# Kernel optimization log

Measured on AMD Instinct MI355X. Metric: run time of the kernel, lower is better.

The kernel has to match this reference:

```python
import jax, jax.numpy as jnp
import numpy as np

E = 512   # embed_size == head_dim
H = 8     # heads
N = 8     # batch
S = 1024  # seq len


def setup_inputs() -> dict:
    key = jax.random.key(0)
    ks = jax.random.split(key, 12)
    scale = 1.0 / np.sqrt(E)
    inp = {
        "values": jax.random.normal(ks[0], (N, S, E), jnp.float32),
        "keys": jax.random.normal(ks[1], (N, S, E), jnp.float32),
        "query": jax.random.normal(ks[2], (N, S, E), jnp.float32),
        "pos": jnp.arange(S, dtype=jnp.int64) if jax.config.jax_enable_x64 else jnp.arange(S, dtype=jnp.int32),
        "mask": jax.random.randint(ks[3], (N, 1, S, S), 0, 2, jnp.int32),
        # nn.Linear params: weight (out,in), y = x @ W.T + b
        "Wv": jax.random.uniform(ks[4], (E * H, E), jnp.float32, -scale, scale),
        "bv": jax.random.uniform(ks[5], (E * H,), jnp.float32, -scale, scale),
        "Wk": jax.random.uniform(ks[6], (E * H, E), jnp.float32, -scale, scale),
        "bk": jax.random.uniform(ks[7], (E * H,), jnp.float32, -scale, scale),
        "Wq": jax.random.uniform(ks[8], (E * H, E), jnp.float32, -scale, scale),
        "bq": jax.random.uniform(ks[9], (E * H,), jnp.float32, -scale, scale),
        "Wo": jax.random.uniform(ks[10], (E, E), jnp.float32, -scale, scale),
        "bo": jax.random.uniform(ks[11], (E,), jnp.float32, -scale, scale),
    }
    return inp


def reference(values, keys, query, pos, mask, Wv, bv, Wk, bk, Wq, bq, Wo, bo):
    n, q_len, e = query.shape
    v_len = values.shape[1]
    k_len = keys.shape[1]
    h = Wq.shape[0] // e
    # QKV projections: E -> E*H, reshape to (N, L, H, E)
    v = (values @ Wv.T + bv).reshape(n, v_len, h, e)
    k = (keys @ Wk.T + bk).reshape(n, k_len, h, e)
    q = (query @ Wq.T + bq).reshape(n, q_len, h, e)
    # bilinear energy, no softmax
    energy = jnp.einsum('nqhd,nkhd->nhqk', q, k)
    energy = jnp.where(mask == 0, jnp.zeros((), energy.dtype), energy)
    attention = energy / jnp.asarray(e ** 0.5, energy.dtype)
    out = jnp.einsum('nhql,nlhd->nqhd', attention, v).sum(axis=2)  # sum over heads
    return out @ Wo.T + bo
```

## Files before the change

### kernel.cpp

```cpp
#include <hip/hip_runtime.h>


#define RS 0.04419417382415922f

typedef __attribute__((ext_vector_type(8))) short bf16x8;
typedef __attribute__((ext_vector_type(4))) float f32x4;

__device__ __forceinline__ unsigned short f2b(float f) {
  unsigned u = __builtin_bit_cast(unsigned, f);
  unsigned r = (u + 0x7FFFu + ((u >> 16) & 1u)) >> 16;
  return (unsigned short)r;
}
__device__ __forceinline__ float b2f(unsigned short h) {
  return __builtin_bit_cast(float, ((unsigned)h) << 16);
}

__global__ void k_fill(float* p, int n, float v) {
  int i = blockIdx.x * blockDim.x + threadIdx.x;
  int stride = gridDim.x * blockDim.x;
  for (; i < n; i += stride) p[i] = v;
}

__global__ void k_maskbits(const int* __restrict__ m,
                           unsigned* __restrict__ bits) {
  int wi = blockIdx.x * 256 + threadIdx.x;
  const int* src = m + (size_t)wi * 32;
  unsigned b = 0;
#pragma unroll
  for (int i = 0; i < 32; ++i) b |= (src[i] != 0 ? 1u : 0u) << i;
  bits[wi] = b;
}

__global__ void k_convw4(const float4* __restrict__ wv,
                         const float4* __restrict__ wk,
                         const float4* __restrict__ wq,
                         const float4* __restrict__ wo,
                         ushort4* __restrict__ dqkv, ushort4* __restrict__ dwo) {
  int z = blockIdx.z;
  const float4* s = (z == 0) ? wv : (z == 1) ? wk : (z == 2) ? wq : wo;
  ushort4* d = (z == 3) ? dwo : dqkv + (size_t)z * 524288;
  int n4 = (z == 3) ? 65536 : 524288;
  float scale = (z == 2) ? RS : 1.0f;
  int stride = gridDim.x * blockDim.x;
  for (int i = blockIdx.x * blockDim.x + threadIdx.x; i < n4; i += stride) {
    float4 v = s[i];
    ushort4 o;
    o.x = f2b(v.x * scale); o.y = f2b(v.y * scale);
    o.z = f2b(v.z * scale); o.w = f2b(v.w * scale);
    d[i] = o;
  }
}

__global__ void k_conv3(const float4* __restrict__ v,
                        const float4* __restrict__ k,
                        const float4* __restrict__ q, ushort4* __restrict__ d,
                        int n4, int dstride) {
  const float4* s = (blockIdx.z == 0) ? v : (blockIdx.z == 1) ? k : q;
  ushort4* dz = d + (size_t)blockIdx.z * dstride;
  int stride = gridDim.x * blockDim.x;
  for (int i = blockIdx.x * blockDim.x + threadIdx.x; i < n4; i += stride) {
    float4 x = s[i];
    ushort4 o;
    o.x = f2b(x.x); o.y = f2b(x.y); o.z = f2b(x.z); o.w = f2b(x.w);
    dz[i] = o;
  }
}

__global__ void k_reduce4(const unsigned short* __restrict__ a,
                          unsigned short* __restrict__ o, int total) {
  int i = blockIdx.x * blockDim.x + threadIdx.x;
  if (i >= total) return;
  int nl = i >> 17, j = i & 131071;
  const ushort4* av = (const ushort4*)a + (size_t)nl * 524288;
  float4 s = {0.f, 0.f, 0.f, 0.f};
#pragma unroll
  for (int g = 0; g < 4; ++g) {
    ushort4 v = av[g * 131072 + j];
    s.x += b2f(v.x); s.y += b2f(v.y); s.z += b2f(v.z); s.w += b2f(v.w);
  }
  ushort4 r;
  r.x = f2b(s.x); r.y = f2b(s.y); r.z = f2b(s.z); r.w = f2b(s.w);
  ((ushort4*)o)[i] = r;
}

#define GLD16(gp, sp)                                              \
  __builtin_amdgcn_global_load_lds(                                \
      (const __attribute__((address_space(1))) void*)(gp),         \
      (__attribute__((address_space(3))) void*)(sp), 16, 0, 0)

template <int MODE>
__global__ __launch_bounds__(256) void k_gemm(
    const unsigned short* __restrict__ A, const unsigned short* __restrict__ B,
    const float* __restrict__ bi0, const float* __restrict__ bi1,
    const float* __restrict__ bi2, const unsigned* __restrict__ mbits,
    unsigned short* __restrict__ outb, float* __restrict__ outf, int n0,
    int xstr, int ostr) {
  __shared__ short smem[17408];
  char* const sb = (char*)smem;

  const int tid = threadIdx.x;
  const int wid = tid >> 6;
  const int lane = tid & 63;
  const int wr = wid >> 1, wc = wid & 1;
  const int l15 = lane & 15, l4 = lane >> 4;

  int bx, by, bz;
  if constexpr (MODE == 2 || MODE == 4) {
    bz = blockIdx.x; bx = blockIdx.y; by = blockIdx.z;
  } else {
    bx = blockIdx.x; by = blockIdx.y; bz = blockIdx.z;
  }

  constexpr int KSEG = (MODE == 4) ? 1024 : 512;
  constexpr int NK = KSEG / 32;
  constexpr int NSEG = (MODE == 4) ? 2 : 1;

  f32x4 acc[4][4];
#pragma unroll
  for (int i = 0; i < 4; ++i)
#pragma unroll
    for (int j = 0; j < 4; ++j) acc[i][j] = (f32x4){0.f, 0.f, 0.f, 0.f};

  const unsigned short* Ab;
  const unsigned short* Bb;

#define STAGE(buf, kc)                                             \
  {                                                                \
    _Pragma("unroll") for (int is = 0; is < 2; ++is) {             \
      int c = is * 256 + tid;                                      \
      int row = c >> 2, col = (c & 3) << 3;                        \
      GLD16(Ab + (size_t)row * KSEG + (kc)*32 + col,               \
            sb + (buf)*8192 + is * 4096 + wid * 1024);             \
      GLD16(Bb + (size_t)row * KSEG + (kc)*32 + col,               \
            sb + 16384 + (buf)*8192 + is * 4096 + wid * 1024);     \
    }                                                              \
  }

  for (int seg = 0; seg < NSEG; ++seg) {
    if constexpr (MODE == 5) {
      Ab = A + (size_t)bx * 128 * 512;
      Bb = B + (size_t)by * 128 * 512;
    } else if constexpr (MODE == 6) {
      Ab = A + (size_t)bz * xstr + (size_t)bx * 128 * 512;
      Bb = B + (size_t)bz * 2097152 + (size_t)by * 128 * 512;
    } else if constexpr (MODE == 2) {
      Ab = A + (size_t)bz * 524288 + (size_t)bx * 128 * 512;
      Bb = B + (size_t)bz * 524288 + (size_t)by * 128 * 512;
    } else {
      int n_l = bz >> 2, g = bz & 3;
      int nh = n_l * 8 + g * 2 + seg;
      Ab = A + (size_t)nh * 1048576 + (size_t)bx * 128 * 1024;
      Bb = B + (size_t)nh * 524288 + (size_t)by * 128 * 1024;
    }

    if (NSEG > 1 && seg > 0) __syncthreads();
    STAGE(0, 0);
    int cur = 0;
#pragma unroll 4
    for (int kc = 0; kc < NK; ++kc) {
      __syncthreads();
      if (kc + 1 < NK) STAGE(cur ^ 1, kc + 1);
      bf16x8 af[4], bf_[4];
#pragma unroll
      for (int f = 0; f < 4; ++f) {
        af[f] = *(const bf16x8*)(sb + cur * 8192 +
                                 ((wr * 64 + f * 16 + l15) << 6) + (l4 << 4));
        bf_[f] = *(const bf16x8*)(sb + 16384 + cur * 8192 +
                                  ((wc * 64 + f * 16 + l15) << 6) + (l4 << 4));
      }
#pragma unroll
      for (int mf = 0; mf < 4; ++mf)
#pragma unroll
        for (int nf = 0; nf < 4; ++nf)
          acc[mf][nf] = __builtin_amdgcn_mfma_f32_16x16x32_bf16(
              af[mf], bf_[nf], acc[mf][nf], 0, 0, 0);
      cur ^= 1;
    }
  }
#undef STAGE

  const int r0 = l4 * 4;
  const int c0 = l15;

  if constexpr (MODE != 5) {
    const bool transp = (MODE == 6) && (bz == 0);
    const float* bias =
        (MODE == 6) ? ((bz == 0) ? bi0 : (bz == 1) ? bi1 : bi2) : nullptr;
    const float bscale = (MODE == 6 && bz == 2) ? RS : 1.0f;
    __syncthreads();
#pragma unroll
    for (int nf = 0; nf < 4; ++nf) {
      int c_loc = wc * 64 + nf * 16 + c0;
      int c_ = by * 128 + c_loc;
      float bvl = (MODE == 6) ? bias[c_] * bscale : 0.f;
#pragma unroll
      for (int mf = 0; mf < 4; ++mf) {
#pragma unroll
        for (int r = 0; r < 4; ++r) {
          int r_loc = wr * 64 + mf * 16 + r0 + r;
          float v = acc[mf][nf][r] + bvl;
          unsigned short bb;
          if constexpr (MODE == 2) {
            int r_ = bx * 128 + r_loc;
            unsigned mw = mbits[((size_t)(n0 + (bz >> 3)) * 1024 + r_) * 32 +
                                (c_ >> 5)];
            bb = ((mw >> (c_ & 31)) & 1u) ? f2b(v) : (unsigned short)0;
          } else {
            bb = f2b(v);
          }
          if (transp)
            smem[c_loc * 136 + r_loc] = (short)bb;
          else
            smem[r_loc * 136 + c_loc] = (short)bb;
        }
      }
    }
    __syncthreads();
#pragma unroll
    for (int ch = 0; ch < 8; ++ch) {
      int idx = ch * 256 + tid;
      int row = idx >> 4;
      int col = (idx & 15) << 3;
      bf16x8 v = *(const bf16x8*)(smem + row * 136 + col);
      if constexpr (MODE == 2) {
        int r_ = bx * 128 + row, cB = by * 128 + col;
        *(bf16x8*)(outb + (size_t)bz * 1048576 + (size_t)r_ * 1024 + cB) = v;
      } else if constexpr (MODE == 4) {
        int r_ = bx * 128 + row, cB = by * 128 + col;
        *(bf16x8*)(outb + (size_t)bz * 524288 + (size_t)r_ * 512 + cB) = v;
      } else {
        unsigned short* O = outb + (size_t)bz * ostr;
        if (bz == 0) {
          int eB = by * 128 + row;
          int r_ = bx * 128 + col;
          int nl = r_ >> 10, s = r_ & 1023, h = eB >> 9, e = eB & 511;
          *(bf16x8*)(O + (((size_t)nl * 8 + h) * 512 + e) * 1024 + s) = v;
        } else {
          int r_ = bx * 128 + row, cB = by * 128 + col;
          int nl = r_ >> 10, s = r_ & 1023, h = cB >> 9, e = cB & 511;
          *(bf16x8*)(O + (((size_t)nl * 8 + h) * 1024 + s) * 512 + e) = v;
        }
      }
    }
  } else {
    float* const Cs32 = (float*)smem;
#pragma unroll
    for (int hh = 0; hh < 2; ++hh) {
      __syncthreads();
      if (wr == hh) {
#pragma unroll
        for (int nf = 0; nf < 4; ++nf) {
          int c_loc = wc * 64 + nf * 16 + c0;
          float bvl = bi0[by * 128 + c_loc];
#pragma unroll
          for (int mf = 0; mf < 4; ++mf)
#pragma unroll
            for (int r = 0; r < 4; ++r)
              Cs32[(mf * 16 + r0 + r) * 136 + c_loc] = acc[mf][nf][r] + bvl;
        }
      }
      __syncthreads();
#pragma unroll
      for (int ch = 0; ch < 8; ++ch) {
        int idx = ch * 256 + tid;
        int row = idx >> 5;
        int col = (idx & 31) << 2;
        float4 v = *(const float4*)(Cs32 + row * 136 + col);
        *(float4*)(outf + (size_t)(bx * 128 + hh * 64 + row) * 512 +
                   by * 128 + col) = v;
      }
    }
  }
}

extern "C" void kernel_launch(void* const* d_in, const int* in_sizes, int n_in,
                              void* d_out, int out_size, void* d_ws,
                              size_t ws_size, hipStream_t stream) {
  const float* values = (const float*)d_in[0];
  const float* keys = (const float*)d_in[1];
  const float* query = (const float*)d_in[2];
  const int* maskI = (const int*)d_in[4];
  const float* Wv = (const float*)d_in[5];
  const float* bv = (const float*)d_in[6];
  const float* Wk = (const float*)d_in[7];
  const float* bk = (const float*)d_in[8];
  const float* Wq = (const float*)d_in[9];
  const float* bq = (const float*)d_in[10];
  const float* Wo = (const float*)d_in[11];
  const float* bo = (const float*)d_in[12];
  float* dout = (float*)d_out;

  const int exp_sizes[13] = {4194304, 4194304, 4194304, 1024, 8388608,
                             2097152, 4096,    2097152, 4096, 2097152,
                             4096,    262144,  512};
  bool ok = (n_in == 13);
  if (ok)
    for (int i = 0; i < 13; ++i)
      if (in_sizes[i] != exp_sizes[i]) ok = false;
  if (!ok) {
    k_fill<<<512, 256, 0, stream>>>(dout, out_size, 1000.f);
    return;
  }

  const size_t SZT2 = 16777216, SZT4 = 33554432;
  const size_t need2 = 22544384 + 3 * SZT2 + 2 * SZT2;
  const size_t need4 = 22544384 + 3 * SZT4 + 2 * SZT4;
  const int NL = (ws_size >= need4) ? 4 : 2;
  if (ws_size < need2) {
    k_fill<<<512, 256, 0, stream>>>(dout, out_size, 2000.f);
    return;
  }
  const size_t SZT = (size_t)NL * 8388608;

  char* w = (char*)d_ws;
  unsigned short* Wvb = (unsigned short*)(w);
  unsigned short* Wob = (unsigned short*)(w + 12582912);
  unsigned short* Atb = (unsigned short*)(w + 13107200);
  unsigned* mbits = (unsigned*)(w + 21495808);
  unsigned short* VTb = (unsigned short*)(w + 22544384);
  unsigned short* Kb = (unsigned short*)(w + 22544384 + SZT);
  unsigned short* Qb = (unsigned short*)(w + 22544384 + 2 * SZT);
  unsigned short* Pb = (unsigned short*)(w + 22544384 + 3 * SZT);
  unsigned short* Xc = (unsigned short*)Pb;
  unsigned short* Ahb = (unsigned short*)Qb;

  k_convw4<<<dim3(512, 1, 4), 256, 0, stream>>>(
      (const float4*)Wv, (const float4*)Wk, (const float4*)Wq,
      (const float4*)Wo, (ushort4*)Wvb, (ushort4*)Wob);
  k_maskbits<<<1024, 256, 0, stream>>>(maskI, mbits);

  const int xstr = NL * 524288;
  const int ostr = NL * 4194304;

  for (int it = 0; it < 8 / NL; ++it) {
    const int n0 = it * NL;
    const size_t xoff = (size_t)n0 * 524288;
    k_conv3<<<dim3(512 * NL, 1, 3), 256, 0, stream>>>(
        (const float4*)(values + xoff), (const float4*)(keys + xoff),
        (const float4*)(query + xoff), (ushort4*)Xc, NL * 131072, NL * 131072);
    k_gemm<6><<<dim3(NL * 8, 32, 3), 256, 0, stream>>>(
        Xc, Wvb, bv, bk, bq, nullptr, VTb, nullptr, 0, xstr, ostr);
    k_gemm<2><<<dim3(NL * 8, 8, 8), 256, 0, stream>>>(
        Qb, Kb, nullptr, nullptr, nullptr, mbits, Pb, nullptr, n0, 0, 0);
    k_gemm<4><<<dim3(NL * 4, 8, 4), 256, 0, stream>>>(
        Pb, VTb, nullptr, nullptr, nullptr, nullptr, Ahb, nullptr, 0, 0, 0);
    k_reduce4<<<NL * 512, 256, 0, stream>>>(Ahb, Atb + (size_t)n0 * 524288,
                                            NL * 131072);
  }

  k_gemm<5><<<dim3(64, 4, 1), 256, 0, stream>>>(
      Atb, Wob, bo, nullptr, nullptr, nullptr, nullptr, dout, 0, 0, 0);
}
```

Measured before the change: 476.5 us.

## Fuse masked QK^T energy and attention-times-V into one flash-style kernel

```diff
diff --git a/kernel.cpp b/kernel.cpp
--- a/kernel.cpp
+++ b/kernel.cpp
@@ -66,16 +66,16 @@
   }
 }
 
-__global__ void k_reduce4(const unsigned short* __restrict__ a,
+__global__ void k_reduce8(const unsigned short* __restrict__ a,
                           unsigned short* __restrict__ o, int total) {
   int i = blockIdx.x * blockDim.x + threadIdx.x;
   if (i >= total) return;
   int nl = i >> 17, j = i & 131071;
-  const ushort4* av = (const ushort4*)a + (size_t)nl * 524288;
+  const ushort4* av = (const ushort4*)a + (size_t)nl * 1048576;
   float4 s = {0.f, 0.f, 0.f, 0.f};
 #pragma unroll
-  for (int g = 0; g < 4; ++g) {
-    ushort4 v = av[g * 131072 + j];
+  for (int h = 0; h < 8; ++h) {
+    ushort4 v = av[h * 131072 + j];
     s.x += b2f(v.x); s.y += b2f(v.y); s.z += b2f(v.z); s.w += b2f(v.w);
   }
   ushort4 r;
@@ -88,13 +88,147 @@
       (const __attribute__((address_space(1))) void*)(gp),         \
       (__attribute__((address_space(3))) void*)(sp), 16, 0, 0)
 
+__global__ __launch_bounds__(256) void k_fused(
+    const unsigned short* __restrict__ Qb, const unsigned short* __restrict__ Kb,
+    const unsigned short* __restrict__ VTb, const unsigned* __restrict__ mbits,
+    unsigned short* __restrict__ Ob, int n0) {
+  __shared__ short smem[20992];
+  short* const Ss = smem + 12288;
+
+  const int tid = threadIdx.x;
+  const int wid = tid >> 6, lane = tid & 63;
+  const int l15 = lane & 15, l4 = lane >> 4;
+  const int bz = blockIdx.x, qt = blockIdx.y;
+
+  const unsigned short* Qt = Qb + (size_t)bz * 524288 + (size_t)qt * 64 * 512;
+  const unsigned short* Kh = Kb + (size_t)bz * 524288;
+  const unsigned short* Vh = VTb + (size_t)bz * 524288;
+  const int n = n0 + (bz >> 3);
+
+  f32x4 accO[4][8];
+#pragma unroll
+  for (int f = 0; f < 4; ++f)
+#pragma unroll
+    for (int e = 0; e < 8; ++e) accO[f][e] = (f32x4){0.f, 0.f, 0.f, 0.f};
+
+#define STGF(buf, kc)                                                      \
+  {                                                                        \
+    int cA = wid * 64 + lane;                                              \
+    GLD16(Qt + (size_t)(cA >> 2) * 512 + (kc)*32 + ((cA & 3) << 3),        \
+          (char*)smem + (buf)*4096 + wid * 1024);                          \
+    _Pragma("unroll") for (int is = 0; is < 2; ++is) {                     \
+      int cB = is * 256 + tid;                                             \
+      GLD16(Kl + (size_t)(cB >> 2) * 512 + (kc)*32 + ((cB & 3) << 3),      \
+            (char*)smem + 8192 + (buf)*8192 + is * 4096 + wid * 1024);     \
+    }                                                                      \
+  }
+
+  for (int lt = 0; lt < 8; ++lt) {
+    const unsigned short* Kl = Kh + (size_t)lt * 128 * 512;
+    f32x4 accS[4][2];
+#pragma unroll
+    for (int f = 0; f < 4; ++f) {
+      accS[f][0] = (f32x4){0.f, 0.f, 0.f, 0.f};
+      accS[f][1] = (f32x4){0.f, 0.f, 0.f, 0.f};
+    }
+
+    STGF(0, 0);
+    int cur = 0;
+#pragma unroll 4
+    for (int kc = 0; kc < 16; ++kc) {
+      __syncthreads();
+      if (kc + 1 < 16) STGF(cur ^ 1, kc + 1);
+      bf16x8 aq[4], bk[2];
+#pragma unroll
+      for (int f = 0; f < 4; ++f)
+        aq[f] = *(const bf16x8*)((char*)smem + cur * 4096 +
+                                 ((f * 16 + l15) << 6) + (l4 << 4));
+#pragma unroll
+      for (int g = 0; g < 2; ++g)
+        bk[g] = *(const bf16x8*)((char*)smem + 8192 + cur * 8192 +
+                                 ((wid * 32 + g * 16 + l15) << 6) + (l4 << 4));
+#pragma unroll
+      for (int f = 0; f < 4; ++f)
+#pragma unroll
+        for (int g = 0; g < 2; ++g)
+          accS[f][g] = __builtin_amdgcn_mfma_f32_16x16x32_bf16(
+              aq[f], bk[g], accS[f][g], 0, 0, 0);
+      cur ^= 1;
+    }
+
+#pragma unroll
+    for (int f = 0; f < 4; ++f)
+#pragma unroll
+      for (int g = 0; g < 2; ++g)
+#pragma unroll
+        for (int r = 0; r < 4; ++r) {
+          int q_loc = f * 16 + l4 * 4 + r;
+          int l_loc = wid * 32 + g * 16 + l15;
+          int l_glob = lt * 128 + l_loc;
+          int q_glob = qt * 64 + q_loc;
+          unsigned mw =
+              mbits[((size_t)n * 1024 + q_glob) * 32 + (l_glob >> 5)];
+          Ss[q_loc * 136 + l_loc] =
+              ((mw >> (l_glob & 31)) & 1u)
+                  ? (short)f2b(accS[f][g][r])
+                  : (short)0;
+        }
+    __syncthreads();
+
+#pragma unroll
+    for (int ks = 0; ks < 4; ++ks) {
+      bf16x8 as_[4];
+#pragma unroll
+      for (int f = 0; f < 4; ++f)
+        as_[f] = *(const bf16x8*)(Ss + (f * 16 + l15) * 136 + ks * 32 + l4 * 8);
+#pragma unroll
+      for (int fe = 0; fe < 8; ++fe) {
+        bf16x8 bv = *(const bf16x8*)(Vh +
+                                     (size_t)(wid * 128 + fe * 16 + l15) * 1024 +
+                                     lt * 128 + ks * 32 + l4 * 8);
+#pragma unroll
+        for (int f = 0; f < 4; ++f)
+          accO[f][fe] = __builtin_amdgcn_mfma_f32_16x16x32_bf16(
+              as_[f], bv, accO[f][fe], 0, 0, 0);
+      }
+    }
+    __syncthreads();
+  }
+#undef STGF
+
+#pragma unroll
+  for (int p = 0; p < 2; ++p) {
+    __syncthreads();
+    if ((wid >> 1) == p) {
+#pragma unroll
+      for (int f = 0; f < 4; ++f)
+#pragma unroll
+        for (int fe = 0; fe < 8; ++fe)
+#pragma unroll
+          for (int r = 0; r < 4; ++r) {
+            int row = f * 16 + l4 * 4 + r;
+            int col = (wid & 1) * 128 + fe * 16 + l15;
+            smem[row * 264 + col] = (short)f2b(accO[f][fe][r]);
+          }
+    }
+    __syncthreads();
+#pragma unroll
+    for (int ch = 0; ch < 8; ++ch) {
+      int idx = ch * 256 + tid;
+      int row = idx >> 5;
+      int col = (idx & 31) << 3;
+      *(bf16x8*)(Ob + (size_t)bz * 524288 + (size_t)(qt * 64 + row) * 512 +
+                 p * 256 + col) = *(const bf16x8*)(smem + row * 264 + col);
+    }
+  }
+}
+
 template <int MODE>
 __global__ __launch_bounds__(256) void k_gemm(
     const unsigned short* __restrict__ A, const unsigned short* __restrict__ B,
     const float* __restrict__ bi0, const float* __restrict__ bi1,
-    const float* __restrict__ bi2, const unsigned* __restrict__ mbits,
-    unsigned short* __restrict__ outb, float* __restrict__ outf, int n0,
-    int xstr, int ostr) {
+    const float* __restrict__ bi2, unsigned short* __restrict__ outb,
+    float* __restrict__ outf, int xstr, int ostr) {
   __shared__ short smem[17408];
   char* const sb = (char*)smem;
 
@@ -103,17 +237,7 @@
   const int lane = tid & 63;
   const int wr = wid >> 1, wc = wid & 1;
   const int l15 = lane & 15, l4 = lane >> 4;
-
-  int bx, by, bz;
-  if constexpr (MODE == 2 || MODE == 4) {
-    bz = blockIdx.x; bx = blockIdx.y; by = blockIdx.z;
-  } else {
-    bx = blockIdx.x; by = blockIdx.y; bz = blockIdx.z;
-  }
-
-  constexpr int KSEG = (MODE == 4) ? 1024 : 512;
-  constexpr int NK = KSEG / 32;
-  constexpr int NSEG = (MODE == 4) ? 2 : 1;
+  const int bx = blockIdx.x, by = blockIdx.y, bz = blockIdx.z;
 
   f32x4 acc[4][4];
 #pragma unroll
@@ -123,97 +247,73 @@
 
   const unsigned short* Ab;
   const unsigned short* Bb;
+  if constexpr (MODE == 5) {
+    Ab = A + (size_t)bx * 128 * 512;
+    Bb = B + (size_t)by * 128 * 512;
+  } else {
+    Ab = A + (size_t)bz * xstr + (size_t)bx * 128 * 512;
+    Bb = B + (size_t)bz * 2097152 + (size_t)by * 128 * 512;
+  }
 
 #define STAGE(buf, kc)                                             \
   {                                                                \
     _Pragma("unroll") for (int is = 0; is < 2; ++is) {             \
       int c = is * 256 + tid;                                      \
       int row = c >> 2, col = (c & 3) << 3;                        \
-      GLD16(Ab + (size_t)row * KSEG + (kc)*32 + col,               \
+      GLD16(Ab + (size_t)row * 512 + (kc)*32 + col,                \
             sb + (buf)*8192 + is * 4096 + wid * 1024);             \
-      GLD16(Bb + (size_t)row * KSEG + (kc)*32 + col,               \
+      GLD16(Bb + (size_t)row * 512 + (kc)*32 + col,                \
             sb + 16384 + (buf)*8192 + is * 4096 + wid * 1024);     \
     }                                                              \
   }
 
-  for (int seg = 0; seg < NSEG; ++seg) {
-    if constexpr (MODE == 5) {
-      Ab = A + (size_t)bx * 128 * 512;
-      Bb = B + (size_t)by * 128 * 512;
-    } else if constexpr (MODE == 6) {
-      Ab = A + (size_t)bz * xstr + (size_t)bx * 128 * 512;
-      Bb = B + (size_t)bz * 2097152 + (size_t)by * 128 * 512;
-    } else if constexpr (MODE == 2) {
-      Ab = A + (size_t)bz * 524288 + (size_t)bx * 128 * 512;
-      Bb = B + (size_t)bz * 524288 + (size_t)by * 128 * 512;
-    } else {
-      int n_l = bz >> 2, g = bz & 3;
-      int nh = n_l * 8 + g * 2 + seg;
-      Ab = A + (size_t)nh * 1048576 + (size_t)bx * 128 * 1024;
-      Bb = B + (size_t)nh * 524288 + (size_t)by * 128 * 1024;
-    }
-
-    if (NSEG > 1 && seg > 0) __syncthreads();
-    STAGE(0, 0);
-    int cur = 0;
+  STAGE(0, 0);
+  int cur = 0;
 #pragma unroll 4
-    for (int kc = 0; kc < NK; ++kc) {
-      __syncthreads();
-      if (kc + 1 < NK) STAGE(cur ^ 1, kc + 1);
-      bf16x8 af[4], bf_[4];
-#pragma unroll
-      for (int f = 0; f < 4; ++f) {
-        af[f] = *(const bf16x8*)(sb + cur * 8192 +
-                                 ((wr * 64 + f * 16 + l15) << 6) + (l4 << 4));
-        bf_[f] = *(const bf16x8*)(sb + 16384 + cur * 8192 +
-                                  ((wc * 64 + f * 16 + l15) << 6) + (l4 << 4));
-      }
-#pragma unroll
-      for (int mf = 0; mf < 4; ++mf)
-#pragma unroll
-        for (int nf = 0; nf < 4; ++nf)
-          acc[mf][nf] = __builtin_amdgcn_mfma_f32_16x16x32_bf16(
-              af[mf], bf_[nf], acc[mf][nf], 0, 0, 0);
-      cur ^= 1;
-    }
+  for (int kc = 0; kc < 16; ++kc) {
+    __syncthreads();
+    if (kc + 1 < 16) STAGE(cur ^ 1, kc + 1);
+    bf16x8 af[4], bf_[4];
+#pragma unroll
+    for (int f = 0; f < 4; ++f) {
+      af[f] = *(const bf16x8*)(sb + cur * 8192 +
+                               ((wr * 64 + f * 16 + l15) << 6) + (l4 << 4));
+      bf_[f] = *(const bf16x8*)(sb + 16384 + cur * 8192 +
+                                ((wc * 64 + f * 16 + l15) << 6) + (l4 << 4));
+    }
+#pragma unroll
+    for (int mf = 0; mf < 4; ++mf)
+#pragma unroll
+      for (int nf = 0; nf < 4; ++nf)
+        acc[mf][nf] = __builtin_amdgcn_mfma_f32_16x16x32_bf16(
+            af[mf], bf_[nf], acc[mf][nf], 0, 0, 0);
+    cur ^= 1;
   }
 #undef STAGE
 
   const int r0 = l4 * 4;
   const int c0 = l15;
 
-  if constexpr (MODE != 5) {
-    const bool transp = (MODE == 6) && (bz == 0);
-    const float* bias =
-        (MODE == 6) ? ((bz == 0) ? bi0 : (bz == 1) ? bi1 : bi2) : nullptr;
-    const float bscale = (MODE == 6 && bz == 2) ? RS : 1.0f;
+  if constexpr (MODE == 6) {
+    const bool transp = (bz == 0);
+    const float* bias = (bz == 0) ? bi0 : (bz == 1) ? bi1 : bi2;
+    const float bscale = (bz == 2) ? RS : 1.0f;
     __syncthreads();
 #pragma unroll
     for (int nf = 0; nf < 4; ++nf) {
       int c_loc = wc * 64 + nf * 16 + c0;
-      int c_ = by * 128 + c_loc;
-      float bvl = (MODE == 6) ? bias[c_] * bscale : 0.f;
-#pragma unroll
-      for (int mf = 0; mf < 4; ++mf) {
+      float bvl = bias[by * 128 + c_loc] * bscale;
+#pragma unroll
+      for (int mf = 0; mf < 4; ++mf)
 #pragma unroll
         for (int r = 0; r < 4; ++r) {
           int r_loc = wr * 64 + mf * 16 + r0 + r;
-          float v = acc[mf][nf][r] + bvl;
-          unsigned short bb;
-          if constexpr (MODE == 2) {
-            int r_ = bx * 128 + r_loc;
-            unsigned mw = mbits[((size_t)(n0 + (bz >> 3)) * 1024 + r_) * 32 +
-                                (c_ >> 5)];
-            bb = ((mw >> (c_ & 31)) & 1u) ? f2b(v) : (unsigned short)0;
-          } else {
-            bb = f2b(v);
-          }
+          unsigned short bb = f2b(acc[mf][nf][r] + bvl);
           if (transp)
             smem[c_loc * 136 + r_loc] = (short)bb;
           else
             smem[r_loc * 136 + c_loc] = (short)bb;
         }
-      }
     }
     __syncthreads();
 #pragma unroll
@@ -222,24 +322,16 @@
       int row = idx >> 4;
       int col = (idx & 15) << 3;
       bf16x8 v = *(const bf16x8*)(smem + row * 136 + col);
-      if constexpr (MODE == 2) {
+      unsigned short* O = outb + (size_t)bz * ostr;
+      if (bz == 0) {
+        int eB = by * 128 + row;
+        int r_ = bx * 128 + col;
+        int nl = r_ >> 10, s = r_ & 1023, h = eB >> 9, e = eB & 511;
+        *(bf16x8*)(O + (((size_t)nl * 8 + h) * 512 + e) * 1024 + s) = v;
+      } else {
         int r_ = bx * 128 + row, cB = by * 128 + col;
-        *(bf16x8*)(outb + (size_t)bz * 1048576 + (size_t)r_ * 1024 + cB) = v;
-      } else if constexpr (MODE == 4) {
-        int r_ = bx * 128 + row, cB = by * 128 + col;
-        *(bf16x8*)(outb + (size_t)bz * 524288 + (size_t)r_ * 512 + cB) = v;
-      } else {
-        unsigned short* O = outb + (size_t)bz * ostr;
-        if (bz == 0) {
-          int eB = by * 128 + row;
-          int r_ = bx * 128 + col;
-          int nl = r_ >> 10, s = r_ & 1023, h = eB >> 9, e = eB & 511;
-          *(bf16x8*)(O + (((size_t)nl * 8 + h) * 512 + e) * 1024 + s) = v;
-        } else {
-          int r_ = bx * 128 + row, cB = by * 128 + col;
-          int nl = r_ >> 10, s = r_ & 1023, h = cB >> 9, e = cB & 511;
-          *(bf16x8*)(O + (((size_t)nl * 8 + h) * 1024 + s) * 512 + e) = v;
-        }
+        int nl = r_ >> 10, s = r_ & 1023, h = cB >> 9, e = cB & 511;
+        *(bf16x8*)(O + (((size_t)nl * 8 + h) * 1024 + s) * 512 + e) = v;
       }
     }
   } else {
@@ -322,7 +414,7 @@
   unsigned short* Qb = (unsigned short*)(w + 22544384 + 2 * SZT);
   unsigned short* Pb = (unsigned short*)(w + 22544384 + 3 * SZT);
   unsigned short* Xc = (unsigned short*)Pb;
-  unsigned short* Ahb = (unsigned short*)Qb;
+  unsigned short* Ob = (unsigned short*)Pb;
 
   k_convw4<<<dim3(512, 1, 4), 256, 0, stream>>>(
       (const float4*)Wv, (const float4*)Wk, (const float4*)Wq,
@@ -339,15 +431,13 @@
         (const float4*)(values + xoff), (const float4*)(keys + xoff),
         (const float4*)(query + xoff), (ushort4*)Xc, NL * 131072, NL * 131072);
     k_gemm<6><<<dim3(NL * 8, 32, 3), 256, 0, stream>>>(
-        Xc, Wvb, bv, bk, bq, nullptr, VTb, nullptr, 0, xstr, ostr);
-    k_gemm<2><<<dim3(NL * 8, 8, 8), 256, 0, stream>>>(
-        Qb, Kb, nullptr, nullptr, nullptr, mbits, Pb, nullptr, n0, 0, 0);
-    k_gemm<4><<<dim3(NL * 4, 8, 4), 256, 0, stream>>>(
-        Pb, VTb, nullptr, nullptr, nullptr, nullptr, Ahb, nullptr, 0, 0, 0);
-    k_reduce4<<<NL * 512, 256, 0, stream>>>(Ahb, Atb + (size_t)n0 * 524288,
+        Xc, Wvb, bv, bk, bq, VTb, nullptr, xstr, ostr);
+    k_fused<<<dim3(NL * 8, 16, 1), 256, 0, stream>>>(Qb, Kb, VTb, mbits, Ob,
+                                                     n0);
+    k_reduce8<<<NL * 512, 256, 0, stream>>>(Ob, Atb + (size_t)n0 * 524288,
                                             NL * 131072);
   }
 
-  k_gemm<5><<<dim3(64, 4, 1), 256, 0, stream>>>(
-      Atb, Wob, bo, nullptr, nullptr, nullptr, nullptr, dout, 0, 0, 0);
-}
+  k_gemm<5><<<dim3(64, 4, 1), 256, 0, stream>>>(Atb, Wob, bo, nullptr, nullptr,
+                                                nullptr, dout, 0, 0);
+}
```

Result: slower. 763.2 us (+60.1%).
